# Kernel optimization log

Measured on AMD Instinct MI355X. Metric: run time of the kernel, lower is better.

Reference implementation:

```python
import jax, jax.numpy as jnp
import numpy as np

HD, IN_SZ, V, OP_SZ = 1024, 1024, 400, 128
B, K, L = 64, 8, 13


def log1mexp(x):
    # log(1 - exp(x)) for x <= 0, numerically stable on both ends
    x = jnp.minimum(x, -1e-38)
    big = x > -0.6931472
    return jnp.where(big,
                     jnp.log(-jnp.expm1(jnp.where(big, x, -1.0))),
                     jnp.log1p(-jnp.exp(jnp.where(big, -1.0, x))))


def compute_log_R(log_p, num_points=1000):
    # Unordered-sample ratios for Plackett-Luce sampling without replacement
    # (Kool et al.). P(S) = (1 - p_S) * int_0^1 u^{-p_S} prod_{j in S}(1 - u^{p_j}) du;
    # the (1 - p_S) prefactor cancels in all ratios. Midpoint rule in log-space.
    p = jnp.exp(log_p)                                   # (B,k)
    p_S = jnp.sum(p, axis=-1, keepdims=True)             # (B,1)
    u = (jnp.arange(num_points, dtype=log_p.dtype) + 0.5) / num_points
    log_u = jnp.log(u)                                   # (N,)
    T = log1mexp(p[:, None, :] * log_u[None, :, None])   # (B,N,k): log(1-u^{p_j})
    base = -p_S * log_u[None, :] + jnp.sum(T, axis=-1)   # (B,N)
    logN = jnp.log(jnp.float32(num_points))
    logI = jax.nn.logsumexp(base, axis=-1) - logN        # (B,)   log I(S)
    logI_s = jax.nn.logsumexp(base[:, :, None] - T, axis=1) - logN   # (B,k)
    log_R_s = logI_s - logI[:, None]
    pair = base[:, :, None, None] - T[:, :, :, None] - T[:, :, None, :]  # (B,N,k,k)
    logI_ss = jax.nn.logsumexp(pair, axis=1) - logN      # (B,k,k)
    kk = log_p.shape[-1]
    log_R_ss = jnp.where(jnp.eye(kk, dtype=bool)[None], 0.0,
                         logI_ss - logI_s[:, :, None])
    return log_R_s, log_R_ss


def gumbel_with_maximum(phi, T, u):
    # Gumbel(phi) sample conditioned on its max over axis 1 equaling T (shape (R,1))
    gmb = -jnp.log(-jnp.log(u * (1.0 - 2e-7) + 1e-7))
    g_phi = phi + gmb
    Z = jnp.max(g_phi, axis=1, keepdims=True)
    v = T - g_phi + log1mexp(g_phi - Z)
    return T - jax.nn.relu(v) - jnp.log1p(jnp.exp(-jnp.abs(v)))


def forward(x_feat, W_in_op, b_in_op, W_ih, W_hh, b_ih, b_hh,
            W_fc1, b_fc1, W_out, b_out, gumbel_u, program_len, k):
    Bn = x_feat.shape[0]
    k = int(k)
    program_len = int(program_len)
    Vn = W_out.shape[0]
    H = W_hh.shape[1]
    R = Bn * k
    # beam-major layout: row j*Bn + i is beam j of batch element i (torch split/cat order)
    x_f = jnp.tile(x_feat, (k, 1))                       # (R, in_sz)
    rows = jnp.arange(R)
    batch_idx = jnp.tile(jnp.arange(Bn), k)
    chunk = jnp.arange(k * Vn) // Vn

    def to_beams(z):  # (R, d) -> (Bn, k*d); = torch.cat(torch.split(z, Bn, 0), 1)
        return z.reshape(k, Bn, -1).transpose(1, 0, 2).reshape(Bn, -1)

    def step(carry, xt):
        h, c, G, logp, temp, samples, outputs, ent_plot, entropy_element = carry
        u_t, t = xt
        inp_op = jax.nn.relu(temp @ W_in_op.T + b_in_op)             # (R,128)
        xin = jnp.concatenate([x_f, inp_op], axis=1)                 # (R,in+128)
        gates = xin @ W_ih.T + b_ih + h @ W_hh.T + b_hh              # (R,4H)
        i_g, f_g, g_g, o_g = jnp.split(gates, 4, axis=1)             # torch LSTM order
        c = jax.nn.sigmoid(f_g) * c + jax.nn.sigmoid(i_g) * jnp.tanh(g_g)
        h = jax.nn.sigmoid(o_g) * jnp.tanh(c)
        hd = jax.nn.relu(h @ W_fc1.T + b_fc1)
        logits = hd @ W_out.T + b_out                                # (R,V)
        log_probs = jax.nn.log_softmax(logits, axis=1)
        probs = jax.nn.softmax(logits, axis=1)
        # ---- stochastic-beam-search SWOR step (selection carries no gradient) ----
        phi = jax.lax.stop_gradient(log_probs + logp)
        g = jax.lax.stop_gradient(gumbel_with_maximum(phi, G, u_t))
        nub = jnp.where(t == 0, 1, k)   # unique parent beams (all identical at t=0)
        g2 = jnp.where(chunk[None, :] < nub, to_beams(g), -jnp.inf)  # (Bn,k*V)
        g_val, index = jax.lax.top_k(g2, k)                          # (Bn,k)
        G_new = g_val.T.reshape(R, 1)
        sample = (index % Vn).T.reshape(R)                           # action ids
        order = (index // Vn).T.reshape(R) * Bn + batch_idx          # parent rows
        log_probs = log_probs[order]
        probs = probs[order]
        logp = logp[order] + log_probs[rows, sample][:, None]
        samples = samples[order].at[:, t].set(sample.astype(samples.dtype))
        outputs = outputs[order].at[:, t].set(log_probs[rows, sample])
        h = h[order]
        c = c[order]
        ent = jnp.sum(log_probs * probs, axis=1, keepdims=True)      # (R,1)
        phi_k = to_beams(logp)                                       # (Bn,k)
        log_R_s, log_R_ss = compute_log_R(phi_k)
        w_p_q = jax.lax.stop_gradient(jnp.exp(phi_k + log_R_s))
        Wsum = jnp.sum(w_p_q, axis=1)
        ws = jnp.sum(w_p_q * to_beams(ent), axis=1)
        ent_plot = ent_plot + ws
        entropy_element = entropy_element + ws / Wsum
        temp = jax.nn.one_hot(sample, Vn + 1, dtype=x_feat.dtype)
        new_carry = (h, c, G_new, logp, temp, samples, outputs, ent_plot, entropy_element)
        return new_carry, (log_R_s, log_R_ss, phi_k)

    z = jnp.zeros
    init = (z((R, H)), z((R, H)), z((R, 1)), z((R, 1)),
            jax.nn.one_hot(jnp.full((R,), Vn), Vn + 1, dtype=x_feat.dtype),
            z((R, program_len)), z((R, program_len)), z((Bn,)), z((Bn,)))
    carry, ys = jax.lax.scan(step, init, (gumbel_u, jnp.arange(program_len)))
    samples, outputs, ent_plot, entropy_element = carry[5], carry[6], carry[7], carry[8]
    log_R_s, log_R_ss, phi_k = ys[0][-1], ys[1][-1], ys[2][-1]
    return (to_beams(outputs), to_beams(samples), entropy_element,
            log_R_s, log_R_ss, phi_k, ent_plot)


def setup_inputs() -> dict:
    key = jax.random.key(0)
    ks = jax.random.split(key, 7)

    def lin(kk, out_f, in_f):  # torch nn.Linear default init
        s = 1.0 / np.sqrt(in_f)
        kw, kb = jax.random.split(kk)
        return (jax.random.uniform(kw, (out_f, in_f), jnp.float32, -s, s),
                jax.random.uniform(kb, (out_f,), jnp.float32, -s, s))

    W_in_op, b_in_op = lin(ks[0], OP_SZ, V + 1)
    W_ih, b_ih = lin(ks[1], 4 * HD, IN_SZ + OP_SZ)
    W_hh, b_hh = lin(ks[2], 4 * HD, HD)
    W_fc1, b_fc1 = lin(ks[3], HD, HD)
    W_out, b_out = lin(ks[4], V, HD)
    x_feat = jax.random.normal(ks[5], (B, IN_SZ), jnp.float32)
    gumbel_u = jax.random.uniform(ks[6], (L, B * K, V), jnp.float32)
    return {"x_feat": x_feat, "W_in_op": W_in_op, "b_in_op": b_in_op,
            "W_ih": W_ih, "W_hh": W_hh, "b_ih": b_ih, "b_hh": b_hh,
            "W_fc1": W_fc1, "b_fc1": b_fc1, "W_out": W_out, "b_out": b_out,
            "gumbel_u": gumbel_u, "program_len": L, "k": K}


def reference(x_feat, W_in_op, b_in_op, W_ih, W_hh, b_ih, b_hh,
              W_fc1, b_fc1, W_out, b_out, gumbel_u, program_len, k):
    return forward(x_feat, W_in_op, b_in_op, W_ih, W_hh, b_ih, b_hh,
                   W_fc1, b_fc1, W_out, b_out, gumbel_u, program_len, k)
```

## Files before the change

kernel.cpp:

```cpp
#include <hip/hip_runtime.h>
#include <hip/hip_bf16.h>
#include <cstdint>

#define RR 512
#define KB_ 8
#define VV 400
#define HD_ 1024
#define GD 4096
#define LL 13
#define BKT 16
#define NPTS 1000
#define OUT_N 18560
#define LDP 68
#define AP 36
#define BP 132

__device__ __constant__ int cPJ[28] = {0,0,0,0,0,0,0,1,1,1,1,1,1,2,2,2,2,2,3,3,3,3,4,4,4,5,5,6};
__device__ __constant__ int cPL[28] = {1,2,3,4,5,6,7,2,3,4,5,6,7,3,4,5,6,7,4,5,6,7,5,6,7,6,7,7};

__device__ __forceinline__ float r9_log1mexp(float x) {
  x = fminf(x, -1e-38f);
  return (x > -0.6931472f) ? logf(-expm1f(x)) : log1pf(-expf(x));
}

__device__ __forceinline__ float r9_sigm(float x) { return 1.f / (1.f + expf(-x)); }

__device__ __forceinline__ int r9_pidx(int j, int l) {
  if (j > l) { int t = j; j = l; l = t; }
  return 9 + (j * (15 - j)) / 2 + (l - j - 1);
}

__device__ __forceinline__ float r9_bmax256(float v, float* red) {
  #pragma unroll
  for (int o = 32; o; o >>= 1) v = fmaxf(v, __shfl_xor(v, o, 64));
  __syncthreads();
  if ((threadIdx.x & 63) == 0) red[threadIdx.x >> 6] = v;
  __syncthreads();
  return fmaxf(fmaxf(red[0], red[1]), fmaxf(red[2], red[3]));
}

__device__ __forceinline__ float r9_bsum256(float v, float* red) {
  #pragma unroll
  for (int o = 32; o; o >>= 1) v += __shfl_xor(v, o, 64);
  __syncthreads();
  if ((threadIdx.x & 63) == 0) red[threadIdx.x >> 6] = v;
  __syncthreads();
  return (red[0] + red[1]) + (red[2] + red[3]);
}

__device__ __forceinline__ void r9_gemm(
    const float* __restrict__ A, int lda,
    const float* __restrict__ W, int ldw,
    int K, int r0, int n0, int nmax,
    float (&acc)[4][4], float (*As)[LDP], float (*Bs)[LDP])
{
  const int tid = threadIdx.x;
  const int la = tid >> 2;
  const int lk = (tid & 3) << 2;
  const int tx = tid & 15, ty = tid >> 4;
  for (int k0 = 0; k0 < K; k0 += BKT) {
    float4 av = *reinterpret_cast<const float4*>(A + (size_t)(r0 + la) * lda + (k0 + lk));
    float4 bv = make_float4(0.f, 0.f, 0.f, 0.f);
    if (n0 + la < nmax)
      bv = *reinterpret_cast<const float4*>(W + (size_t)(n0 + la) * ldw + (k0 + lk));
    __syncthreads();
    As[lk + 0][la] = av.x; As[lk + 1][la] = av.y; As[lk + 2][la] = av.z; As[lk + 3][la] = av.w;
    Bs[lk + 0][la] = bv.x; Bs[lk + 1][la] = bv.y; Bs[lk + 2][la] = bv.z; Bs[lk + 3][la] = bv.w;
    __syncthreads();
    #pragma unroll
    for (int kk = 0; kk < BKT; ++kk) {
      float4 a = *reinterpret_cast<const float4*>(&As[kk][ty * 4]);
      float4 b = *reinterpret_cast<const float4*>(&Bs[kk][tx * 4]);
      float ar[4] = {a.x, a.y, a.z, a.w};
      float br[4] = {b.x, b.y, b.z, b.w};
      #pragma unroll
      for (int i = 0; i < 4; ++i)
        #pragma unroll
        for (int j = 0; j < 4; ++j)
          acc[i][j] = fmaf(ar[i], br[j], acc[i][j]);
    }
  }
}

__global__ __launch_bounds__(256) void r9_wszero(float* h0, float* c0, float* Gv,
                                                 float* logp0, float* accum) {
  int idx = blockIdx.x * 256 + threadIdx.x;
  if (idx < RR * HD_) { h0[idx] = 0.f; c0[idx] = 0.f; }
  if (idx < RR) { Gv[idx] = 0.f; logp0[idx] = 0.f; }
  if (idx < 128) accum[idx] = 0.f;
}

__global__ __launch_bounds__(256) void r9_flag(float* dout) {
  int idx = blockIdx.x * 256 + threadIdx.x;
  if (idx < OUT_N) dout[idx] = (idx == 6656) ? 20000.0f : 0.0f;
}

__global__ __launch_bounds__(256) void r9_xfb(const float* __restrict__ xf,
                                              const float* __restrict__ Wih,
                                              const float* __restrict__ bih,
                                              const float* __restrict__ bhh,
                                              float* __restrict__ xfb) {
  __shared__ __align__(16) float As[BKT][LDP];
  __shared__ __align__(16) float Bs[BKT][LDP];
  float acc[4][4] = {};
  int n0 = blockIdx.x * 64;
  r9_gemm(xf, 1024, Wih, 1152, 1024, 0, n0, 1 << 30, acc, As, Bs);
  int tx = threadIdx.x & 15, ty = threadIdx.x >> 4;
  #pragma unroll
  for (int i = 0; i < 4; ++i)
    #pragma unroll
    for (int j = 0; j < 4; ++j) {
      int r = ty * 4 + i, c = n0 + tx * 4 + j;
      xfb[(size_t)r * GD + c] = acc[i][j] + bih[c] + bhh[c];
    }
}

__global__ __launch_bounds__(256) void r9_glstm(
    const float* __restrict__ hprev,
    const float* __restrict__ Whh, const float* __restrict__ Wih,
    const float* __restrict__ Wio, const float* __restrict__ bio,
    const int* __restrict__ s_arr, const int* __restrict__ o_arr, int t,
    float* __restrict__ gates)
{
  __shared__ __align__(16) float As[BKT][AP];
  __shared__ __align__(16) float Bs[BKT][BP];
  float acc[4][4] = {};
  const int tid = threadIdx.x;
  const int c0 = blockIdx.x * 128;
  const int r0 = blockIdx.y * 32;
  const int g  = blockIdx.z;
  const int a_r = tid >> 3;
  const int a_k = (tid & 7) * 2;
  const int b_r = tid >> 1;
  const int b_k = (tid & 1) * 8;
  const int tx = tid & 31, ty = tid >> 5;
  const int arow = r0 + a_r;
  const int asrc = (t == 0) ? arow : o_arr[(size_t)(t - 1) * RR + arow];
  const int s_row = (t == 0) ? 400 : s_arr[(size_t)(t - 1) * RR + arow];
  const float* Arow  = hprev + (size_t)asrc * HD_;
  const float* BrowW = Whh + (size_t)(g * 1024 + c0 + b_r) * HD_;
  for (int k0 = 0; k0 < HD_; k0 += BKT) {
    float2 av = *reinterpret_cast<const float2*>(Arow + k0 + a_k);
    float4 b0 = *reinterpret_cast<const float4*>(BrowW + k0 + b_k);
    float4 b1 = *reinterpret_cast<const float4*>(BrowW + k0 + b_k + 4);
    __syncthreads();
    As[a_k][a_r] = av.x; As[a_k + 1][a_r] = av.y;
    Bs[b_k + 0][b_r] = b0.x; Bs[b_k + 1][b_r] = b0.y;
    Bs[b_k + 2][b_r] = b0.z; Bs[b_k + 3][b_r] = b0.w;
    Bs[b_k + 4][b_r] = b1.x; Bs[b_k + 5][b_r] = b1.y;
    Bs[b_k + 6][b_r] = b1.z; Bs[b_k + 7][b_r] = b1.w;
    __syncthreads();
    #pragma unroll
    for (int kk = 0; kk < BKT; ++kk) {
      float4 a = *reinterpret_cast<const float4*>(&As[kk][ty * 4]);
      float4 b = *reinterpret_cast<const float4*>(&Bs[kk][tx * 4]);
      float ar[4] = {a.x, a.y, a.z, a.w};
      float br[4] = {b.x, b.y, b.z, b.w};
      #pragma unroll
      for (int i = 0; i < 4; ++i)
        #pragma unroll
        for (int j = 0; j < 4; ++j)
          acc[i][j] = fmaf(ar[i], br[j], acc[i][j]);
    }
  }
  const float* BrowI = Wih + (size_t)(g * 1024 + c0 + b_r) * 1152 + 1024;
  for (int k0 = 0; k0 < 128; k0 += BKT) {
    int m0 = k0 + a_k;
    float a0 = fmaxf(Wio[(size_t)m0 * 401 + s_row] + bio[m0], 0.f);
    float a1 = fmaxf(Wio[(size_t)(m0 + 1) * 401 + s_row] + bio[m0 + 1], 0.f);
    float4 b0 = *reinterpret_cast<const float4*>(BrowI + k0 + b_k);
    float4 b1 = *reinterpret_cast<const float4*>(BrowI + k0 + b_k + 4);
    __syncthreads();
    As[a_k][a_r] = a0; As[a_k + 1][a_r] = a1;
    Bs[b_k + 0][b_r] = b0.x; Bs[b_k + 1][b_r] = b0.y;
    Bs[b_k + 2][b_r] = b0.z; Bs[b_k + 3][b_r] = b0.w;
    Bs[b_k + 4][b_r] = b1.x; Bs[b_k + 5][b_r] = b1.y;
    Bs[b_k + 6][b_r] = b1.z; Bs[b_k + 7][b_r] = b1.w;
    __syncthreads();
    #pragma unroll
    for (int kk = 0; kk < BKT; ++kk) {
      float4 a = *reinterpret_cast<const float4*>(&As[kk][ty * 4]);
      float4 b = *reinterpret_cast<const float4*>(&Bs[kk][tx * 4]);
      float ar[4] = {a.x, a.y, a.z, a.w};
      float br[4] = {b.x, b.y, b.z, b.w};
      #pragma unroll
      for (int i = 0; i < 4; ++i)
        #pragma unroll
        for (int j = 0; j < 4; ++j)
          acc[i][j] = fmaf(ar[i], br[j], acc[i][j]);
    }
  }
  #pragma unroll
  for (int i = 0; i < 4; ++i)
    #pragma unroll
    for (int j = 0; j < 4; ++j)
      gates[(size_t)(r0 + ty * 4 + i) * GD + g * 1024 + c0 + tx * 4 + j] = acc[i][j];
}

__global__ __launch_bounds__(256) void r9_lstm(const float* gates, const float* xfb,
                                               const float* cprev, const int* o_arr, int t,
                                               float* cout, float* hout) {
  int idx = blockIdx.x * 256 + threadIdx.x;
  int r = idx >> 10, n = idx & 1023;
  int src = (t == 0) ? r : o_arr[(size_t)(t - 1) * RR + r];
  const float* g = gates + (size_t)r * GD;
  const float* xb = xfb + (size_t)(r & 63) * GD;
  float gi = g[n] + xb[n];
  float gf = g[1024 + n] + xb[1024 + n];
  float gg = g[2048 + n] + xb[2048 + n];
  float go = g[3072 + n] + xb[3072 + n];
  float cp = cprev[(size_t)src * HD_ + n];
  float c = r9_sigm(gf) * cp + r9_sigm(gi) * tanhf(gg);
  cout[idx] = c;
  hout[idx] = r9_sigm(go) * tanhf(c);
}

__global__ __launch_bounds__(256) void r9_fc1(const float* h, const float* W1, float* hdp) {
  __shared__ __align__(16) float As[BKT][LDP];
  __shared__ __align__(16) float Bs[BKT][LDP];
  float acc[4][4] = {};
  int n0 = blockIdx.x * 64, r0 = blockIdx.y * 64, z = blockIdx.z;
  r9_gemm(h + z * 512, HD_, W1 + z * 512, HD_, 512, r0, n0, 1 << 30, acc, As, Bs);
  float* dst = hdp + (size_t)z * RR * HD_;
  int tx = threadIdx.x & 15, ty = threadIdx.x >> 4;
  #pragma unroll
  for (int i = 0; i < 4; ++i)
    #pragma unroll
    for (int j = 0; j < 4; ++j)
      dst[(size_t)(r0 + ty * 4 + i) * HD_ + n0 + tx * 4 + j] = acc[i][j];
}

__global__ __launch_bounds__(256) void r9_fc1c(const float* hdp, const float* b1, float* hd) {
  int idx = blockIdx.x * 256 + threadIdx.x;
  hd[idx] = fmaxf(hdp[idx] + hdp[RR * HD_ + idx] + b1[idx & 1023], 0.f);
}

__global__ __launch_bounds__(256) void r9_out(const float* hd, const float* Wo, float* outp) {
  __shared__ __align__(16) float As[BKT][LDP];
  __shared__ __align__(16) float Bs[BKT][LDP];
  float acc[4][4] = {};
  int n0 = blockIdx.x * 64, r0 = blockIdx.y * 64, z = blockIdx.z;
  r9_gemm(hd + z * 256, HD_, Wo + z * 256, HD_, 256, r0, n0, VV, acc, As, Bs);
  float* dst = outp + (size_t)z * RR * VV;
  int tx = threadIdx.x & 15, ty = threadIdx.x >> 4;
  #pragma unroll
  for (int i = 0; i < 4; ++i)
    #pragma unroll
    for (int j = 0; j < 4; ++j) {
      int c = n0 + tx * 4 + j;
      if (c < VV) dst[(size_t)(r0 + ty * 4 + i) * VV + c] = acc[i][j];
    }
}

__global__ __launch_bounds__(256) void r9_soft(const float* outp, const float* bo,
                                               const float* logp_in, const float* Gv,
                                               const float* gum, float* lp, float* gb,
                                               float* entold) {
  __shared__ float red[4];
  int r = blockIdx.x, tid = threadIdx.x;
  bool v1 = (tid + 256) < VV;
  size_t off0 = (size_t)r * VV + tid;
  float l0 = outp[off0] + outp[RR * VV + off0] + outp[2 * RR * VV + off0]
           + outp[3 * RR * VV + off0] + bo[tid];
  float l1 = -INFINITY;
  if (v1) {
    size_t off1 = off0 + 256;
    l1 = outp[off1] + outp[RR * VV + off1] + outp[2 * RR * VV + off1]
       + outp[3 * RR * VV + off1] + bo[tid + 256];
  }
  float m = r9_bmax256(fmaxf(l0, l1), red);
  float e0 = expf(l0 - m), e1 = v1 ? expf(l1 - m) : 0.f;
  float s = r9_bsum256(e0 + e1, red);
  float ls = logf(s);
  float lp0 = l0 - m - ls, lp1 = l1 - m - ls;
  float ent = lp0 * expf(lp0) + (v1 ? lp1 * expf(lp1) : 0.f);
  ent = r9_bsum256(ent, red);
  if (tid == 0) entold[r] = ent;
  float lpr = logp_in[r];
  const float* ur = gum + (size_t)r * VV;
  float gp0, gp1 = -INFINITY;
  { float u = ur[tid];
    gp0 = lp0 + lpr - logf(-logf(u * (1.f - 2e-7f) + 1e-7f)); }
  if (v1) { float u = ur[tid + 256];
            gp1 = lp1 + lpr - logf(-logf(u * (1.f - 2e-7f) + 1e-7f)); }
  float Z = r9_bmax256(fmaxf(gp0, gp1), red);
  float T = Gv[r];
  int i = r & 63, j = r >> 6;
  float* gbr = gb + (size_t)i * (KB_ * VV) + j * VV;
  {
    float vv = T - gp0 + r9_log1mexp(gp0 - Z);
    gbr[tid] = T - fmaxf(vv, 0.f) - log1pf(expf(-fabsf(vv)));
    lp[(size_t)r * VV + tid] = lp0;
  }
  if (v1) {
    float vv = T - gp1 + r9_log1mexp(gp1 - Z);
    gbr[tid + 256] = T - fmaxf(vv, 0.f) - log1pf(expf(-fabsf(vv)));
    lp[(size_t)r * VV + tid + 256] = lp1;
  }
}

__device__ __forceinline__ unsigned long long r9_pack(float v, int c) {
  unsigned u = __float_as_uint(v);
  u = (u & 0x80000000u) ? ~u : (u | 0x80000000u);
  return ((unsigned long long)u << 32) | (unsigned)(0xFFFFFFFFu - (unsigned)c);
}

__global__ __launch_bounds__(256) void r9_topk(const float* gb, int t, float* Gv,
                                               int* s_t, int* o_t, const float* lp,
                                               const float* logp_in, float* logp_out,
                                               const float* entold, float* entbm,
                                               float* lv_t) {
  __shared__ unsigned long long keys[KB_ * VV];
  __shared__ unsigned long long wbest[4];
  __shared__ unsigned long long selK[KB_];
  int i = blockIdx.x, tid = threadIdx.x;
  int lane = tid & 63, wid = tid >> 6;
  int limit = (t == 0) ? VV : KB_ * VV;
  for (int c = tid; c < limit; c += 256)
    keys[c] = r9_pack(gb[(size_t)i * (KB_ * VV) + c], c);
  __syncthreads();
  for (int it = 0; it < KB_; ++it) {
    unsigned long long b = 0ull;
    for (int c = tid; c < limit; c += 256) {
      unsigned long long k = keys[c];
      b = (k > b) ? k : b;
    }
    #pragma unroll
    for (int o = 32; o; o >>= 1) {
      unsigned long long x = __shfl_xor(b, o, 64);
      b = (x > b) ? x : b;
    }
    if (lane == 0) wbest[wid] = b;
    __syncthreads();
    unsigned long long g = wbest[0];
    g = (wbest[1] > g) ? wbest[1] : g;
    g = (wbest[2] > g) ? wbest[2] : g;
    g = (wbest[3] > g) ? wbest[3] : g;
    if (tid == 0) {
      int csel = (int)(0xFFFFFFFFu - (unsigned)(g & 0xFFFFFFFFu));
      keys[csel] = 0ull;
      selK[it] = g;
    }
    __syncthreads();
  }
  if (tid < KB_) {
    unsigned long long g = selK[tid];
    unsigned x = (unsigned)(g >> 32);
    x = (x & 0x80000000u) ? (x & 0x7FFFFFFFu) : ~x;
    float v = __uint_as_float(x);
    int c = (int)(0xFFFFFFFFu - (unsigned)(g & 0xFFFFFFFFu));
    int r = tid * 64 + i;
    int s = c % VV;
    int o = (c / VV) * 64 + i;
    Gv[r] = v;
    s_t[r] = s;
    o_t[r] = o;
    float lv = lp[(size_t)o * VV + s];
    logp_out[r] = logp_in[o] + lv;
    entbm[r] = entold[o];
    lv_t[r] = lv;
  }
}

__global__ __launch_bounds__(256) void r9_logR(const float* logp_new, const float* entbm,
                                               float* accum, float* dout, int last) {
  __shared__ float Tm[KB_][NPTS];
  __shared__ float base[NPTS];
  __shared__ float phi[KB_], pj[KB_];
  __shared__ float res[37];
  int i = blockIdx.x, tid = threadIdx.x;
  int lane = tid & 63, wid = tid >> 6;
  if (tid < KB_) { float ph = logp_new[tid * 64 + i]; phi[tid] = ph; pj[tid] = expf(ph); }
  __syncthreads();
  float pS = ((pj[0] + pj[1]) + (pj[2] + pj[3])) + ((pj[4] + pj[5]) + (pj[6] + pj[7]));
  for (int n = tid; n < NPTS; n += 256) {
    float lu = logf((n + 0.5f) * (1.0f / NPTS));
    float b = -pS * lu;
    #pragma unroll
    for (int j = 0; j < KB_; ++j) {
      float tv = r9_log1mexp(pj[j] * lu);
      Tm[j][n] = tv; b += tv;
    }
    base[n] = b;
  }
  __syncthreads();
  const float logN = 6.9077552789821f;
  for (int ridx = wid; ridx < 37; ridx += 4) {
    int jj = -1, ll = -1;
    if (ridx >= 1 && ridx < 9) jj = ridx - 1;
    else if (ridx >= 9) { jj = cPJ[ridx - 9]; ll = cPL[ridx - 9]; }
    float mx = -INFINITY;
    for (int n = lane; n < NPTS; n += 64) {
      float v = base[n];
      if (jj >= 0) v -= Tm[jj][n];
      if (ll >= 0) v -= Tm[ll][n];
      mx = fmaxf(mx, v);
    }
    #pragma unroll
    for (int o = 32; o; o >>= 1) mx = fmaxf(mx, __shfl_xor(mx, o, 64));
    float sm = 0.f;
    for (int n = lane; n < NPTS; n += 64) {
      float v = base[n];
      if (jj >= 0) v -= Tm[jj][n];
      if (ll >= 0) v -= Tm[ll][n];
      sm += expf(v - mx);
    }
    #pragma unroll
    for (int o = 32; o; o >>= 1) sm += __shfl_xor(sm, o, 64);
    if (lane == 0) res[ridx] = mx + logf(sm) - logN;
  }
  __syncthreads();
  if (tid == 0) {
    float logI = res[0];
    float Wsum = 0.f, ws = 0.f;
    #pragma unroll
    for (int j = 0; j < KB_; ++j) {
      float lRs = res[1 + j] - logI;
      float wj = expf(phi[j] + lRs);
      Wsum += wj;
      ws += wj * entbm[j * 64 + i];
    }
    accum[i] += ws;
    accum[64 + i] += ws / Wsum;
    if (last) {
      for (int j = 0; j < KB_; ++j) {
        dout[13376 + i * 8 + j] = res[1 + j] - logI;
        dout[17984 + i * 8 + j] = phi[j];
        for (int l = 0; l < KB_; ++l) {
          float v = (l == j) ? 0.f : (res[r9_pidx(j, l)] - res[1 + j]);
          dout[13888 + i * 64 + j * 8 + l] = v;
        }
      }
    }
  }
}

__global__ __launch_bounds__(512) void r9_final(const float* lv_arr, const int* s_arr,
                                                const int* o_arr, const float* accum,
                                                float* dout) {
  int r = threadIdx.x;
  int i = r & 63, j = r >> 6;
  float vals[LL]; int svs[LL];
  int a = r;
  for (int tt = LL - 1; tt >= 0; --tt) {
    vals[tt] = lv_arr[tt * RR + a];
    svs[tt]  = s_arr[tt * RR + a];
    a = o_arr[tt * RR + a];
  }
  #pragma unroll
  for (int tt = 0; tt < LL; ++tt) {
    dout[i * 104 + j * 13 + tt] = vals[tt];
    dout[6656 + i * 104 + j * 13 + tt] = (float)svs[tt];
  }
  if (r < 64) {
    dout[13312 + r] = accum[64 + r];
    dout[18496 + r] = accum[r];
  }
}

extern "C" void kernel_launch(void* const* d_in, const int* in_sizes, int n_in,
                              void* d_out, int out_size, void* d_ws, size_t ws_size,
                              hipStream_t stream) {
  const float* x_feat  = (const float*)d_in[0];
  const float* W_in_op = (const float*)d_in[1];
  const float* b_in_op = (const float*)d_in[2];
  const float* W_ih    = (const float*)d_in[3];
  const float* W_hh    = (const float*)d_in[4];
  const float* b_ih    = (const float*)d_in[5];
  const float* b_hh    = (const float*)d_in[6];
  const float* W_fc1   = (const float*)d_in[7];
  const float* b_fc1   = (const float*)d_in[8];
  const float* W_out   = (const float*)d_in[9];
  const float* b_out   = (const float*)d_in[10];
  const float* gum     = (const float*)d_in[11];
  float* out           = (float*)d_out;

  float* W = (float*)d_ws;
  size_t o = 0;
  float* lv_arr = W + o; o += (size_t)LL * RR;
  float* Gv     = W + o; o += RR;
  float* logpb0 = W + o; o += RR;
  float* logpb1 = W + o; o += RR;
  float* entold = W + o; o += RR;
  float* entbm  = W + o; o += RR;
  float* accum  = W + o; o += 128;
  int* s_arr = (int*)(W + o); o += (size_t)LL * RR;
  int* o_arr = (int*)(W + o); o += (size_t)LL * RR;
  float* xfb    = W + o; o += (size_t)64 * GD;
  float* gates  = W + o; o += (size_t)RR * GD;
  float* lp     = W + o; o += (size_t)RR * VV;
  float* gb     = W + o; o += (size_t)RR * VV;
  float* h2[2]; h2[0] = W + o; o += (size_t)RR * HD_; h2[1] = W + o; o += (size_t)RR * HD_;
  float* c2[2]; c2[0] = W + o; o += (size_t)RR * HD_; c2[1] = W + o; o += (size_t)RR * HD_;
  float* hd     = W + o; o += (size_t)RR * HD_;
  size_t needed_bytes = o * sizeof(float);
  float* logpb[2] = {logpb0, logpb1};
  float* hdp  = gates;
  float* outp = gates;

  if (ws_size < needed_bytes) {
    r9_flag<<<(OUT_N + 255) / 256, 256, 0, stream>>>(out);
    return;
  }

  r9_wszero<<<2048, 256, 0, stream>>>(h2[0], c2[0], Gv, logpb[0], accum);
  r9_xfb<<<64, 256, 0, stream>>>(x_feat, W_ih, b_ih, b_hh, xfb);

  for (int t = 0; t < LL; ++t) {
    int pi = t & 1, po = pi ^ 1;
    r9_glstm<<<dim3(8, 16, 4), 256, 0, stream>>>(h2[pi], W_hh, W_ih, W_in_op, b_in_op,
                                                 s_arr, o_arr, t, gates);
    r9_lstm<<<2048, 256, 0, stream>>>(gates, xfb, c2[pi], o_arr, t, c2[po], h2[po]);
    r9_fc1<<<dim3(16, 8, 2), 256, 0, stream>>>(h2[po], W_fc1, hdp);
    r9_fc1c<<<2048, 256, 0, stream>>>(hdp, b_fc1, hd);
    r9_out<<<dim3(7, 8, 4), 256, 0, stream>>>(hd, W_out, outp);
    r9_soft<<<512, 256, 0, stream>>>(outp, b_out, logpb[pi], Gv,
                                     gum + (size_t)t * RR * VV, lp, gb, entold);
    r9_topk<<<64, 256, 0, stream>>>(gb, t, Gv, s_arr + (size_t)t * RR,
                                    o_arr + (size_t)t * RR, lp, logpb[pi], logpb[po],
                                    entold, entbm, lv_arr + (size_t)t * RR);
    r9_logR<<<64, 256, 0, stream>>>(logpb[po], entbm, accum, out, (t == LL - 1) ? 1 : 0);
  }
  r9_final<<<1, 512, 0, stream>>>(lv_arr, s_arr, o_arr, accum, out);
}
```

Measured before the change: 2.758 ms.

## Retile GEMMs to 4x8 microtiles and fuse softmax, top-k and logR per batch

The LSTM-gate, fc1 and output GEMMs move to 128-thread blocks with 4x8 register microtiles, vectorised A loads and float4 stores. The fc1 bias+ReLU combine is folded into the output GEMM's A-load, removing a separate kernel and its buffer. Softmax, Gumbel sampling, top-k selection and the log-R integration are merged into one kernel per batch element that keeps log-probs and Gumbel keys in shared memory. This cuts launches and global round-trips, but the fused kernel runs only 64 blocks, and the new GEMM tiling halves threads per block.

```diff
diff --git a/kernel.cpp b/kernel.cpp
--- a/kernel.cpp
+++ b/kernel.cpp
@@ -12,57 +12,62 @@
 #define NPTS 1000
 #define OUT_N 18560
 #define LDP 68
-#define AP 36
-#define BP 132
 
 __device__ __constant__ int cPJ[28] = {0,0,0,0,0,0,0,1,1,1,1,1,1,2,2,2,2,2,3,3,3,3,4,4,4,5,5,6};
 __device__ __constant__ int cPL[28] = {1,2,3,4,5,6,7,2,3,4,5,6,7,3,4,5,6,7,4,5,6,7,5,6,7,6,7,7};
 
-__device__ __forceinline__ float r9_log1mexp(float x) {
+__device__ __forceinline__ float rA_log1mexp(float x) {
   x = fminf(x, -1e-38f);
   return (x > -0.6931472f) ? logf(-expm1f(x)) : log1pf(-expf(x));
 }
 
-__device__ __forceinline__ float r9_sigm(float x) { return 1.f / (1.f + expf(-x)); }
-
-__device__ __forceinline__ int r9_pidx(int j, int l) {
+__device__ __forceinline__ float rA_sigm(float x) { return 1.f / (1.f + expf(-x)); }
+
+__device__ __forceinline__ int rA_pidx(int j, int l) {
   if (j > l) { int t = j; j = l; l = t; }
   return 9 + (j * (15 - j)) / 2 + (l - j - 1);
 }
 
-__device__ __forceinline__ float r9_bmax256(float v, float* red) {
+__device__ __forceinline__ float rA_wmax(float v) {
   #pragma unroll
   for (int o = 32; o; o >>= 1) v = fmaxf(v, __shfl_xor(v, o, 64));
-  __syncthreads();
-  if ((threadIdx.x & 63) == 0) red[threadIdx.x >> 6] = v;
-  __syncthreads();
-  return fmaxf(fmaxf(red[0], red[1]), fmaxf(red[2], red[3]));
-}
-
-__device__ __forceinline__ float r9_bsum256(float v, float* red) {
+  return v;
+}
+
+__device__ __forceinline__ float rA_wsum(float v) {
   #pragma unroll
   for (int o = 32; o; o >>= 1) v += __shfl_xor(v, o, 64);
-  __syncthreads();
-  if ((threadIdx.x & 63) == 0) red[threadIdx.x >> 6] = v;
-  __syncthreads();
-  return (red[0] + red[1]) + (red[2] + red[3]);
-}
-
-__device__ __forceinline__ void r9_gemm(
-    const float* __restrict__ A, int lda,
-    const float* __restrict__ W, int ldw,
-    int K, int r0, int n0, int nmax,
-    float (&acc)[4][4], float (*As)[LDP], float (*Bs)[LDP])
-{
+  return v;
+}
+
+__global__ __launch_bounds__(256) void rA_wszero(float* h0, float* c0, float* Gv,
+                                                 float* logp0, float* accum) {
+  int idx = blockIdx.x * 256 + threadIdx.x;
+  if (idx < RR * HD_) { h0[idx] = 0.f; c0[idx] = 0.f; }
+  if (idx < RR) { Gv[idx] = 0.f; logp0[idx] = 0.f; }
+  if (idx < 128) accum[idx] = 0.f;
+}
+
+__global__ __launch_bounds__(256) void rA_flag(float* dout) {
+  int idx = blockIdx.x * 256 + threadIdx.x;
+  if (idx < OUT_N) dout[idx] = (idx == 6656) ? 20000.0f : 0.0f;
+}
+
+__global__ __launch_bounds__(256) void rA_xfb(const float* __restrict__ xf,
+                                              const float* __restrict__ Wih,
+                                              const float* __restrict__ bih,
+                                              const float* __restrict__ bhh,
+                                              float* __restrict__ xfb) {
+  __shared__ __align__(16) float As[BKT][LDP];
+  __shared__ __align__(16) float Bs[BKT][LDP];
+  float acc[4][4] = {};
   const int tid = threadIdx.x;
-  const int la = tid >> 2;
-  const int lk = (tid & 3) << 2;
+  const int n0 = blockIdx.x * 64;
+  const int la = tid >> 2, lk = (tid & 3) << 2;
   const int tx = tid & 15, ty = tid >> 4;
-  for (int k0 = 0; k0 < K; k0 += BKT) {
-    float4 av = *reinterpret_cast<const float4*>(A + (size_t)(r0 + la) * lda + (k0 + lk));
-    float4 bv = make_float4(0.f, 0.f, 0.f, 0.f);
-    if (n0 + la < nmax)
-      bv = *reinterpret_cast<const float4*>(W + (size_t)(n0 + la) * ldw + (k0 + lk));
+  for (int k0 = 0; k0 < 1024; k0 += BKT) {
+    float4 av = *reinterpret_cast<const float4*>(xf + (size_t)la * 1024 + k0 + lk);
+    float4 bv = *reinterpret_cast<const float4*>(Wih + (size_t)(n0 + la) * 1152 + k0 + lk);
     __syncthreads();
     As[lk + 0][la] = av.x; As[lk + 1][la] = av.y; As[lk + 2][la] = av.z; As[lk + 3][la] = av.w;
     Bs[lk + 0][la] = bv.x; Bs[lk + 1][la] = bv.y; Bs[lk + 2][la] = bv.z; Bs[lk + 3][la] = bv.w;
@@ -80,32 +85,6 @@
           acc[i][j] = fmaf(ar[i], br[j], acc[i][j]);
     }
   }
-}
-
-__global__ __launch_bounds__(256) void r9_wszero(float* h0, float* c0, float* Gv,
-                                                 float* logp0, float* accum) {
-  int idx = blockIdx.x * 256 + threadIdx.x;
-  if (idx < RR * HD_) { h0[idx] = 0.f; c0[idx] = 0.f; }
-  if (idx < RR) { Gv[idx] = 0.f; logp0[idx] = 0.f; }
-  if (idx < 128) accum[idx] = 0.f;
-}
-
-__global__ __launch_bounds__(256) void r9_flag(float* dout) {
-  int idx = blockIdx.x * 256 + threadIdx.x;
-  if (idx < OUT_N) dout[idx] = (idx == 6656) ? 20000.0f : 0.0f;
-}
-
-__global__ __launch_bounds__(256) void r9_xfb(const float* __restrict__ xf,
-                                              const float* __restrict__ Wih,
-                                              const float* __restrict__ bih,
-                                              const float* __restrict__ bhh,
-                                              float* __restrict__ xfb) {
-  __shared__ __align__(16) float As[BKT][LDP];
-  __shared__ __align__(16) float Bs[BKT][LDP];
-  float acc[4][4] = {};
-  int n0 = blockIdx.x * 64;
-  r9_gemm(xf, 1024, Wih, 1152, 1024, 0, n0, 1 << 30, acc, As, Bs);
-  int tx = threadIdx.x & 15, ty = threadIdx.x >> 4;
   #pragma unroll
   for (int i = 0; i < 4; ++i)
     #pragma unroll
@@ -115,89 +94,92 @@
     }
 }
 
-__global__ __launch_bounds__(256) void r9_glstm(
+__global__ __launch_bounds__(128) void rA_glstm(
     const float* __restrict__ hprev,
     const float* __restrict__ Whh, const float* __restrict__ Wih,
     const float* __restrict__ Wio, const float* __restrict__ bio,
     const int* __restrict__ s_arr, const int* __restrict__ o_arr, int t,
     float* __restrict__ gates)
 {
-  __shared__ __align__(16) float As[BKT][AP];
-  __shared__ __align__(16) float Bs[BKT][BP];
-  float acc[4][4] = {};
+  __shared__ __align__(16) float As[BKT][LDP];
+  __shared__ __align__(16) float Bs[BKT][LDP];
+  float acc[4][8] = {};
   const int tid = threadIdx.x;
-  const int c0 = blockIdx.x * 128;
-  const int r0 = blockIdx.y * 32;
+  const int c0 = blockIdx.x * 64;
+  const int r0 = blockIdx.y * 64;
   const int g  = blockIdx.z;
-  const int a_r = tid >> 3;
-  const int a_k = (tid & 7) * 2;
-  const int b_r = tid >> 1;
-  const int b_k = (tid & 1) * 8;
-  const int tx = tid & 31, ty = tid >> 5;
-  const int arow = r0 + a_r;
+  const int sr = tid >> 1;
+  const int sk = (tid & 1) * 8;
+  const int tx = tid & 7, ty = tid >> 3;
+  const int arow = r0 + sr;
   const int asrc = (t == 0) ? arow : o_arr[(size_t)(t - 1) * RR + arow];
   const int s_row = (t == 0) ? 400 : s_arr[(size_t)(t - 1) * RR + arow];
-  const float* Arow  = hprev + (size_t)asrc * HD_;
-  const float* BrowW = Whh + (size_t)(g * 1024 + c0 + b_r) * HD_;
+  const float* Arow = hprev + (size_t)asrc * HD_;
+  const float* Brow = Whh + (size_t)(g * 1024 + c0 + sr) * HD_;
   for (int k0 = 0; k0 < HD_; k0 += BKT) {
-    float2 av = *reinterpret_cast<const float2*>(Arow + k0 + a_k);
-    float4 b0 = *reinterpret_cast<const float4*>(BrowW + k0 + b_k);
-    float4 b1 = *reinterpret_cast<const float4*>(BrowW + k0 + b_k + 4);
-    __syncthreads();
-    As[a_k][a_r] = av.x; As[a_k + 1][a_r] = av.y;
-    Bs[b_k + 0][b_r] = b0.x; Bs[b_k + 1][b_r] = b0.y;
-    Bs[b_k + 2][b_r] = b0.z; Bs[b_k + 3][b_r] = b0.w;
-    Bs[b_k + 4][b_r] = b1.x; Bs[b_k + 5][b_r] = b1.y;
-    Bs[b_k + 6][b_r] = b1.z; Bs[b_k + 7][b_r] = b1.w;
+    float4 a0 = *reinterpret_cast<const float4*>(Arow + k0 + sk);
+    float4 a1 = *reinterpret_cast<const float4*>(Arow + k0 + sk + 4);
+    float4 b0 = *reinterpret_cast<const float4*>(Brow + k0 + sk);
+    float4 b1 = *reinterpret_cast<const float4*>(Brow + k0 + sk + 4);
+    __syncthreads();
+    As[sk + 0][sr] = a0.x; As[sk + 1][sr] = a0.y; As[sk + 2][sr] = a0.z; As[sk + 3][sr] = a0.w;
+    As[sk + 4][sr] = a1.x; As[sk + 5][sr] = a1.y; As[sk + 6][sr] = a1.z; As[sk + 7][sr] = a1.w;
+    Bs[sk + 0][sr] = b0.x; Bs[sk + 1][sr] = b0.y; Bs[sk + 2][sr] = b0.z; Bs[sk + 3][sr] = b0.w;
+    Bs[sk + 4][sr] = b1.x; Bs[sk + 5][sr] = b1.y; Bs[sk + 6][sr] = b1.z; Bs[sk + 7][sr] = b1.w;
     __syncthreads();
     #pragma unroll
     for (int kk = 0; kk < BKT; ++kk) {
       float4 a = *reinterpret_cast<const float4*>(&As[kk][ty * 4]);
-      float4 b = *reinterpret_cast<const float4*>(&Bs[kk][tx * 4]);
+      float4 bA = *reinterpret_cast<const float4*>(&Bs[kk][tx * 8]);
+      float4 bB = *reinterpret_cast<const float4*>(&Bs[kk][tx * 8 + 4]);
       float ar[4] = {a.x, a.y, a.z, a.w};
-      float br[4] = {b.x, b.y, b.z, b.w};
+      float br[8] = {bA.x, bA.y, bA.z, bA.w, bB.x, bB.y, bB.z, bB.w};
       #pragma unroll
       for (int i = 0; i < 4; ++i)
         #pragma unroll
-        for (int j = 0; j < 4; ++j)
+        for (int j = 0; j < 8; ++j)
           acc[i][j] = fmaf(ar[i], br[j], acc[i][j]);
     }
   }
-  const float* BrowI = Wih + (size_t)(g * 1024 + c0 + b_r) * 1152 + 1024;
+  const float* BrowI = Wih + (size_t)(g * 1024 + c0 + sr) * 1152 + 1024;
   for (int k0 = 0; k0 < 128; k0 += BKT) {
-    int m0 = k0 + a_k;
-    float a0 = fmaxf(Wio[(size_t)m0 * 401 + s_row] + bio[m0], 0.f);
-    float a1 = fmaxf(Wio[(size_t)(m0 + 1) * 401 + s_row] + bio[m0 + 1], 0.f);
-    float4 b0 = *reinterpret_cast<const float4*>(BrowI + k0 + b_k);
-    float4 b1 = *reinterpret_cast<const float4*>(BrowI + k0 + b_k + 4);
-    __syncthreads();
-    As[a_k][a_r] = a0; As[a_k + 1][a_r] = a1;
-    Bs[b_k + 0][b_r] = b0.x; Bs[b_k + 1][b_r] = b0.y;
-    Bs[b_k + 2][b_r] = b0.z; Bs[b_k + 3][b_r] = b0.w;
-    Bs[b_k + 4][b_r] = b1.x; Bs[b_k + 5][b_r] = b1.y;
-    Bs[b_k + 6][b_r] = b1.z; Bs[b_k + 7][b_r] = b1.w;
+    float av[8];
+    #pragma unroll
+    for (int m = 0; m < 8; ++m) {
+      int mm = k0 + sk + m;
+      av[m] = fmaxf(Wio[(size_t)mm * 401 + s_row] + bio[mm], 0.f);
+    }
+    float4 b0 = *reinterpret_cast<const float4*>(BrowI + k0 + sk);
+    float4 b1 = *reinterpret_cast<const float4*>(BrowI + k0 + sk + 4);
+    __syncthreads();
+    #pragma unroll
+    for (int m = 0; m < 8; ++m) As[sk + m][sr] = av[m];
+    Bs[sk + 0][sr] = b0.x; Bs[sk + 1][sr] = b0.y; Bs[sk + 2][sr] = b0.z; Bs[sk + 3][sr] = b0.w;
+    Bs[sk + 4][sr] = b1.x; Bs[sk + 5][sr] = b1.y; Bs[sk + 6][sr] = b1.z; Bs[sk + 7][sr] = b1.w;
     __syncthreads();
     #pragma unroll
     for (int kk = 0; kk < BKT; ++kk) {
       float4 a = *reinterpret_cast<const float4*>(&As[kk][ty * 4]);
-      float4 b = *reinterpret_cast<const float4*>(&Bs[kk][tx * 4]);
+      float4 bA = *reinterpret_cast<const float4*>(&Bs[kk][tx * 8]);
+      float4 bB = *reinterpret_cast<const float4*>(&Bs[kk][tx * 8 + 4]);
       float ar[4] = {a.x, a.y, a.z, a.w};
-      float br[4] = {b.x, b.y, b.z, b.w};
+      float br[8] = {bA.x, bA.y, bA.z, bA.w, bB.x, bB.y, bB.z, bB.w};
       #pragma unroll
       for (int i = 0; i < 4; ++i)
         #pragma unroll
-        for (int j = 0; j < 4; ++j)
+        for (int j = 0; j < 8; ++j)
           acc[i][j] = fmaf(ar[i], br[j], acc[i][j]);
     }
   }
   #pragma unroll
-  for (int i = 0; i < 4; ++i)
-    #pragma unroll
-    for (int j = 0; j < 4; ++j)
-      gates[(size_t)(r0 + ty * 4 + i) * GD + g * 1024 + c0 + tx * 4 + j] = acc[i][j];
-}
-
-__global__ __launch_bounds__(256) void r9_lstm(const float* gates, const float* xfb,
+  for (int i = 0; i < 4; ++i) {
+    float* dst = gates + (size_t)(r0 + ty * 4 + i) * GD + g * 1024 + c0 + tx * 8;
+    *reinterpret_cast<float4*>(dst) = make_float4(acc[i][0], acc[i][1], acc[i][2], acc[i][3]);
+    *reinterpret_cast<float4*>(dst + 4) = make_float4(acc[i][4], acc[i][5], acc[i][6], acc[i][7]);
+  }
+}
+
+__global__ __launch_bounds__(256) void rA_lstm(const float* gates, const float* xfb,
                                                const float* cprev, const int* o_arr, int t,
                                                float* cout, float* hout) {
   int idx = blockIdx.x * 256 + threadIdx.x;
@@ -210,119 +192,204 @@
   float gg = g[2048 + n] + xb[2048 + n];
   float go = g[3072 + n] + xb[3072 + n];
   float cp = cprev[(size_t)src * HD_ + n];
-  float c = r9_sigm(gf) * cp + r9_sigm(gi) * tanhf(gg);
+  float c = rA_sigm(gf) * cp + rA_sigm(gi) * tanhf(gg);
   cout[idx] = c;
-  hout[idx] = r9_sigm(go) * tanhf(c);
-}
-
-__global__ __launch_bounds__(256) void r9_fc1(const float* h, const float* W1, float* hdp) {
+  hout[idx] = rA_sigm(go) * tanhf(c);
+}
+
+__global__ __launch_bounds__(128) void rA_fc1(const float* __restrict__ h,
+                                              const float* __restrict__ W1, float* hdp) {
   __shared__ __align__(16) float As[BKT][LDP];
   __shared__ __align__(16) float Bs[BKT][LDP];
-  float acc[4][4] = {};
-  int n0 = blockIdx.x * 64, r0 = blockIdx.y * 64, z = blockIdx.z;
-  r9_gemm(h + z * 512, HD_, W1 + z * 512, HD_, 512, r0, n0, 1 << 30, acc, As, Bs);
-  float* dst = hdp + (size_t)z * RR * HD_;
-  int tx = threadIdx.x & 15, ty = threadIdx.x >> 4;
-  #pragma unroll
-  for (int i = 0; i < 4; ++i)
-    #pragma unroll
-    for (int j = 0; j < 4; ++j)
-      dst[(size_t)(r0 + ty * 4 + i) * HD_ + n0 + tx * 4 + j] = acc[i][j];
-}
-
-__global__ __launch_bounds__(256) void r9_fc1c(const float* hdp, const float* b1, float* hd) {
-  int idx = blockIdx.x * 256 + threadIdx.x;
-  hd[idx] = fmaxf(hdp[idx] + hdp[RR * HD_ + idx] + b1[idx & 1023], 0.f);
-}
-
-__global__ __launch_bounds__(256) void r9_out(const float* hd, const float* Wo, float* outp) {
+  float acc[4][8] = {};
+  const int tid = threadIdx.x;
+  const int n0 = blockIdx.x * 64, r0 = blockIdx.y * 64, z = blockIdx.z;
+  const int sr = tid >> 1, sk = (tid & 1) * 8;
+  const int tx = tid & 7, ty = tid >> 3;
+  const float* Arow = h + (size_t)(r0 + sr) * HD_ + z * 512;
+  const float* Brow = W1 + (size_t)(n0 + sr) * HD_ + z * 512;
+  for (int k0 = 0; k0 < 512; k0 += BKT) {
+    float4 a0 = *reinterpret_cast<const float4*>(Arow + k0 + sk);
+    float4 a1 = *reinterpret_cast<const float4*>(Arow + k0 + sk + 4);
+    float4 b0 = *reinterpret_cast<const float4*>(Brow + k0 + sk);
+    float4 b1 = *reinterpret_cast<const float4*>(Brow + k0 + sk + 4);
+    __syncthreads();
+    As[sk + 0][sr] = a0.x; As[sk + 1][sr] = a0.y; As[sk + 2][sr] = a0.z; As[sk + 3][sr] = a0.w;
+    As[sk + 4][sr] = a1.x; As[sk + 5][sr] = a1.y; As[sk + 6][sr] = a1.z; As[sk + 7][sr] = a1.w;
+    Bs[sk + 0][sr] = b0.x; Bs[sk + 1][sr] = b0.y; Bs[sk + 2][sr] = b0.z; Bs[sk + 3][sr] = b0.w;
+    Bs[sk + 4][sr] = b1.x; Bs[sk + 5][sr] = b1.y; Bs[sk + 6][sr] = b1.z; Bs[sk + 7][sr] = b1.w;
+    __syncthreads();
+    #pragma unroll
+    for (int kk = 0; kk < BKT; ++kk) {
+      float4 a = *reinterpret_cast<const float4*>(&As[kk][ty * 4]);
+      float4 bA = *reinterpret_cast<const float4*>(&Bs[kk][tx * 8]);
+      float4 bB = *reinterpret_cast<const float4*>(&Bs[kk][tx * 8 + 4]);
+      float ar[4] = {a.x, a.y, a.z, a.w};
+      float br[8] = {bA.x, bA.y, bA.z, bA.w, bB.x, bB.y, bB.z, bB.w};
+      #pragma unroll
+      for (int i = 0; i < 4; ++i)
+        #pragma unroll
+        for (int j = 0; j < 8; ++j)
+          acc[i][j] = fmaf(ar[i], br[j], acc[i][j]);
+    }
+  }
+  float* base = hdp + (size_t)z * RR * HD_;
+  #pragma unroll
+  for (int i = 0; i < 4; ++i) {
+    float* dst = base + (size_t)(r0 + ty * 4 + i) * HD_ + n0 + tx * 8;
+    *reinterpret_cast<float4*>(dst) = make_float4(acc[i][0], acc[i][1], acc[i][2], acc[i][3]);
+    *reinterpret_cast<float4*>(dst + 4) = make_float4(acc[i][4], acc[i][5], acc[i][6], acc[i][7]);
+  }
+}
+
+__global__ __launch_bounds__(128) void rA_out(const float* __restrict__ hdp,
+                                              const float* __restrict__ b1,
+                                              const float* __restrict__ Wo, float* outp) {
   __shared__ __align__(16) float As[BKT][LDP];
   __shared__ __align__(16) float Bs[BKT][LDP];
-  float acc[4][4] = {};
-  int n0 = blockIdx.x * 64, r0 = blockIdx.y * 64, z = blockIdx.z;
-  r9_gemm(hd + z * 256, HD_, Wo + z * 256, HD_, 256, r0, n0, VV, acc, As, Bs);
-  float* dst = outp + (size_t)z * RR * VV;
-  int tx = threadIdx.x & 15, ty = threadIdx.x >> 4;
+  float acc[4][8] = {};
+  const int tid = threadIdx.x;
+  const int n0 = blockIdx.x * 64, r0 = blockIdx.y * 64, z = blockIdx.z;
+  const int sr = tid >> 1, sk = (tid & 1) * 8;
+  const int tx = tid & 7, ty = tid >> 3;
+  const size_t arow_off = (size_t)(r0 + sr) * HD_ + z * 256;
+  const int bcol = n0 + sr;
+  const float* Brow = Wo + (size_t)bcol * HD_ + z * 256;
+  for (int k0 = 0; k0 < 256; k0 += BKT) {
+    float av[8];
+    #pragma unroll
+    for (int m = 0; m < 8; ++m) {
+      int kg = z * 256 + k0 + sk + m;
+      av[m] = fmaxf(hdp[arow_off + k0 + sk + m] + hdp[RR * HD_ + arow_off + k0 + sk + m]
+                    + b1[kg], 0.f);
+    }
+    float4 b0 = make_float4(0.f, 0.f, 0.f, 0.f), b1v = b0;
+    if (bcol < VV) {
+      b0  = *reinterpret_cast<const float4*>(Brow + k0 + sk);
+      b1v = *reinterpret_cast<const float4*>(Brow + k0 + sk + 4);
+    }
+    __syncthreads();
+    #pragma unroll
+    for (int m = 0; m < 8; ++m) As[sk + m][sr] = av[m];
+    Bs[sk + 0][sr] = b0.x; Bs[sk + 1][sr] = b0.y; Bs[sk + 2][sr] = b0.z; Bs[sk + 3][sr] = b0.w;
+    Bs[sk + 4][sr] = b1v.x; Bs[sk + 5][sr] = b1v.y; Bs[sk + 6][sr] = b1v.z; Bs[sk + 7][sr] = b1v.w;
+    __syncthreads();
+    #pragma unroll
+    for (int kk = 0; kk < BKT; ++kk) {
+      float4 a = *reinterpret_cast<const float4*>(&As[kk][ty * 4]);
+      float4 bA = *reinterpret_cast<const float4*>(&Bs[kk][tx * 8]);
+      float4 bB = *reinterpret_cast<const float4*>(&Bs[kk][tx * 8 + 4]);
+      float ar[4] = {a.x, a.y, a.z, a.w};
+      float br[8] = {bA.x, bA.y, bA.z, bA.w, bB.x, bB.y, bB.z, bB.w};
+      #pragma unroll
+      for (int i = 0; i < 4; ++i)
+        #pragma unroll
+        for (int j = 0; j < 8; ++j)
+          acc[i][j] = fmaf(ar[i], br[j], acc[i][j]);
+    }
+  }
+  float* base = outp + (size_t)z * RR * VV;
   #pragma unroll
   for (int i = 0; i < 4; ++i)
     #pragma unroll
-    for (int j = 0; j < 4; ++j) {
-      int c = n0 + tx * 4 + j;
-      if (c < VV) dst[(size_t)(r0 + ty * 4 + i) * VV + c] = acc[i][j];
-    }
-}
-
-__global__ __launch_bounds__(256) void r9_soft(const float* outp, const float* bo,
-                                               const float* logp_in, const float* Gv,
-                                               const float* gum, float* lp, float* gb,
-                                               float* entold) {
-  __shared__ float red[4];
-  int r = blockIdx.x, tid = threadIdx.x;
-  bool v1 = (tid + 256) < VV;
-  size_t off0 = (size_t)r * VV + tid;
-  float l0 = outp[off0] + outp[RR * VV + off0] + outp[2 * RR * VV + off0]
-           + outp[3 * RR * VV + off0] + bo[tid];
-  float l1 = -INFINITY;
-  if (v1) {
-    size_t off1 = off0 + 256;
-    l1 = outp[off1] + outp[RR * VV + off1] + outp[2 * RR * VV + off1]
-       + outp[3 * RR * VV + off1] + bo[tid + 256];
-  }
-  float m = r9_bmax256(fmaxf(l0, l1), red);
-  float e0 = expf(l0 - m), e1 = v1 ? expf(l1 - m) : 0.f;
-  float s = r9_bsum256(e0 + e1, red);
-  float ls = logf(s);
-  float lp0 = l0 - m - ls, lp1 = l1 - m - ls;
-  float ent = lp0 * expf(lp0) + (v1 ? lp1 * expf(lp1) : 0.f);
-  ent = r9_bsum256(ent, red);
-  if (tid == 0) entold[r] = ent;
-  float lpr = logp_in[r];
-  const float* ur = gum + (size_t)r * VV;
-  float gp0, gp1 = -INFINITY;
-  { float u = ur[tid];
-    gp0 = lp0 + lpr - logf(-logf(u * (1.f - 2e-7f) + 1e-7f)); }
-  if (v1) { float u = ur[tid + 256];
-            gp1 = lp1 + lpr - logf(-logf(u * (1.f - 2e-7f) + 1e-7f)); }
-  float Z = r9_bmax256(fmaxf(gp0, gp1), red);
-  float T = Gv[r];
-  int i = r & 63, j = r >> 6;
-  float* gbr = gb + (size_t)i * (KB_ * VV) + j * VV;
-  {
-    float vv = T - gp0 + r9_log1mexp(gp0 - Z);
-    gbr[tid] = T - fmaxf(vv, 0.f) - log1pf(expf(-fabsf(vv)));
-    lp[(size_t)r * VV + tid] = lp0;
-  }
-  if (v1) {
-    float vv = T - gp1 + r9_log1mexp(gp1 - Z);
-    gbr[tid + 256] = T - fmaxf(vv, 0.f) - log1pf(expf(-fabsf(vv)));
-    lp[(size_t)r * VV + tid + 256] = lp1;
-  }
-}
-
-__device__ __forceinline__ unsigned long long r9_pack(float v, int c) {
+    for (int j = 0; j < 8; ++j) {
+      int c = n0 + tx * 8 + j;
+      if (c < VV) base[(size_t)(r0 + ty * 4 + i) * VV + c] = acc[i][j];
+    }
+}
+
+__device__ __forceinline__ unsigned long long rA_pack(float v, int c) {
   unsigned u = __float_as_uint(v);
   u = (u & 0x80000000u) ? ~u : (u | 0x80000000u);
   return ((unsigned long long)u << 32) | (unsigned)(0xFFFFFFFFu - (unsigned)c);
 }
 
-__global__ __launch_bounds__(256) void r9_topk(const float* gb, int t, float* Gv,
-                                               int* s_t, int* o_t, const float* lp,
-                                               const float* logp_in, float* logp_out,
-                                               const float* entold, float* entbm,
-                                               float* lv_t) {
-  __shared__ unsigned long long keys[KB_ * VV];
-  __shared__ unsigned long long wbest[4];
-  __shared__ unsigned long long selK[KB_];
-  int i = blockIdx.x, tid = threadIdx.x;
-  int lane = tid & 63, wid = tid >> 6;
+__global__ __launch_bounds__(256) void rA_smax(
+    const float* __restrict__ outp, const float* __restrict__ bo,
+    const float* __restrict__ logp_in, float* logp_out, float* Gv,
+    const float* __restrict__ gum, int* s_t, int* o_t, float* lv_t,
+    float* accum, float* dout, int t, int last)
+{
+  __shared__ __align__(16) float shbuf[9000];
+  __shared__ float entold8[KB_], phi8[KB_], entb8[KB_], pj8[KB_];
+  __shared__ float res[37];
+  __shared__ unsigned long long wbest[4], selK[KB_];
+  float* gk  = shbuf;
+  float* lpl = shbuf + 3200;
+  const int i = blockIdx.x, tid = threadIdx.x;
+  const int lane = tid & 63, wid = tid >> 6;
+
+  for (int rl = wid; rl < KB_; rl += 4) {
+    int r = rl * 64 + i;
+    float lv_[7];
+    float m = -INFINITY;
+    #pragma unroll
+    for (int ch = 0; ch < 7; ++ch) {
+      int n = ch * 64 + lane;
+      float l = -INFINITY;
+      if (n < VV) {
+        size_t off = (size_t)r * VV + n;
+        l = outp[off] + outp[RR * VV + off] + outp[2 * RR * VV + off]
+          + outp[3 * RR * VV + off] + bo[n];
+      }
+      lv_[ch] = l;
+      m = fmaxf(m, l);
+    }
+    m = rA_wmax(m);
+    float ssum = 0.f;
+    #pragma unroll
+    for (int ch = 0; ch < 7; ++ch) {
+      int n = ch * 64 + lane;
+      if (n < VV) ssum += expf(lv_[ch] - m);
+    }
+    ssum = rA_wsum(ssum);
+    float ls = logf(ssum);
+    float ent = 0.f;
+    #pragma unroll
+    for (int ch = 0; ch < 7; ++ch) {
+      int n = ch * 64 + lane;
+      if (n < VV) {
+        float lp = lv_[ch] - m - ls;
+        lpl[rl * VV + n] = lp;
+        ent += lp * expf(lp);
+        lv_[ch] = lp;
+      }
+    }
+    ent = rA_wsum(ent);
+    if (lane == 0) entold8[rl] = ent;
+    float lpr = logp_in[r];
+    const float* ur = gum + (size_t)r * VV;
+    float gp_[7];
+    float Z = -INFINITY;
+    #pragma unroll
+    for (int ch = 0; ch < 7; ++ch) {
+      int n = ch * 64 + lane;
+      float gp = -INFINITY;
+      if (n < VV) {
+        float u = ur[n];
+        gp = lv_[ch] + lpr - logf(-logf(u * (1.f - 2e-7f) + 1e-7f));
+      }
+      gp_[ch] = gp;
+      Z = fmaxf(Z, gp);
+    }
+    Z = rA_wmax(Z);
+    float T = Gv[r];
+    #pragma unroll
+    for (int ch = 0; ch < 7; ++ch) {
+      int n = ch * 64 + lane;
+      if (n < VV) {
+        float vv = T - gp_[ch] + rA_log1mexp(gp_[ch] - Z);
+        gk[rl * VV + n] = T - fmaxf(vv, 0.f) - log1pf(expf(-fabsf(vv)));
+      }
+    }
+  }
+  __syncthreads();
+
   int limit = (t == 0) ? VV : KB_ * VV;
-  for (int c = tid; c < limit; c += 256)
-    keys[c] = r9_pack(gb[(size_t)i * (KB_ * VV) + c], c);
-  __syncthreads();
   for (int it = 0; it < KB_; ++it) {
     unsigned long long b = 0ull;
     for (int c = tid; c < limit; c += 256) {
-      unsigned long long k = keys[c];
+      unsigned long long k = rA_pack(gk[c], c);
       b = (k > b) ? k : b;
     }
     #pragma unroll
@@ -338,11 +405,12 @@
     g = (wbest[3] > g) ? wbest[3] : g;
     if (tid == 0) {
       int csel = (int)(0xFFFFFFFFu - (unsigned)(g & 0xFFFFFFFFu));
-      keys[csel] = 0ull;
+      gk[csel] = -INFINITY;
       selK[it] = g;
     }
     __syncthreads();
   }
+
   if (tid < KB_) {
     unsigned long long g = selK[tid];
     unsigned x = (unsigned)(g >> 32);
@@ -351,34 +419,30 @@
     int c = (int)(0xFFFFFFFFu - (unsigned)(g & 0xFFFFFFFFu));
     int r = tid * 64 + i;
     int s = c % VV;
-    int o = (c / VV) * 64 + i;
+    int jp = c / VV;
+    int o = jp * 64 + i;
     Gv[r] = v;
     s_t[r] = s;
     o_t[r] = o;
-    float lv = lp[(size_t)o * VV + s];
-    logp_out[r] = logp_in[o] + lv;
-    entbm[r] = entold[o];
+    float lv = lpl[jp * VV + s];
+    float ph = logp_in[o] + lv;
+    logp_out[r] = ph;
     lv_t[r] = lv;
-  }
-}
-
-__global__ __launch_bounds__(256) void r9_logR(const float* logp_new, const float* entbm,
-                                               float* accum, float* dout, int last) {
-  __shared__ float Tm[KB_][NPTS];
-  __shared__ float base[NPTS];
-  __shared__ float phi[KB_], pj[KB_];
-  __shared__ float res[37];
-  int i = blockIdx.x, tid = threadIdx.x;
-  int lane = tid & 63, wid = tid >> 6;
-  if (tid < KB_) { float ph = logp_new[tid * 64 + i]; phi[tid] = ph; pj[tid] = expf(ph); }
+    phi8[tid] = ph;
+    pj8[tid] = expf(ph);
+    entb8[tid] = entold8[jp];
+  }
   __syncthreads();
-  float pS = ((pj[0] + pj[1]) + (pj[2] + pj[3])) + ((pj[4] + pj[5]) + (pj[6] + pj[7]));
+
+  float (*Tm)[NPTS] = reinterpret_cast<float (*)[NPTS]>(shbuf);
+  float* base = shbuf + 8000;
+  float pS = ((pj8[0] + pj8[1]) + (pj8[2] + pj8[3])) + ((pj8[4] + pj8[5]) + (pj8[6] + pj8[7]));
   for (int n = tid; n < NPTS; n += 256) {
     float lu = logf((n + 0.5f) * (1.0f / NPTS));
     float b = -pS * lu;
     #pragma unroll
     for (int j = 0; j < KB_; ++j) {
-      float tv = r9_log1mexp(pj[j] * lu);
+      float tv = rA_log1mexp(pj8[j] * lu);
       Tm[j][n] = tv; b += tv;
     }
     base[n] = b;
@@ -396,8 +460,7 @@
       if (ll >= 0) v -= Tm[ll][n];
       mx = fmaxf(mx, v);
     }
-    #pragma unroll
-    for (int o = 32; o; o >>= 1) mx = fmaxf(mx, __shfl_xor(mx, o, 64));
+    mx = rA_wmax(mx);
     float sm = 0.f;
     for (int n = lane; n < NPTS; n += 64) {
       float v = base[n];
@@ -405,8 +468,7 @@
       if (ll >= 0) v -= Tm[ll][n];
       sm += expf(v - mx);
     }
-    #pragma unroll
-    for (int o = 32; o; o >>= 1) sm += __shfl_xor(sm, o, 64);
+    sm = rA_wsum(sm);
     if (lane == 0) res[ridx] = mx + logf(sm) - logN;
   }
   __syncthreads();
@@ -416,18 +478,18 @@
     #pragma unroll
     for (int j = 0; j < KB_; ++j) {
       float lRs = res[1 + j] - logI;
-      float wj = expf(phi[j] + lRs);
+      float wj = expf(phi8[j] + lRs);
       Wsum += wj;
-      ws += wj * entbm[j * 64 + i];
+      ws += wj * entb8[j];
     }
     accum[i] += ws;
     accum[64 + i] += ws / Wsum;
     if (last) {
       for (int j = 0; j < KB_; ++j) {
         dout[13376 + i * 8 + j] = res[1 + j] - logI;
-        dout[17984 + i * 8 + j] = phi[j];
+        dout[17984 + i * 8 + j] = phi8[j];
         for (int l = 0; l < KB_; ++l) {
-          float v = (l == j) ? 0.f : (res[r9_pidx(j, l)] - res[1 + j]);
+          float v = (l == j) ? 0.f : (res[rA_pidx(j, l)] - res[1 + j]);
           dout[13888 + i * 64 + j * 8 + l] = v;
         }
       }
@@ -435,7 +497,7 @@
   }
 }
 
-__global__ __launch_bounds__(512) void r9_final(const float* lv_arr, const int* s_arr,
+__global__ __launch_bounds__(512) void rA_final(const float* lv_arr, const int* s_arr,
                                                 const int* o_arr, const float* accum,
                                                 float* dout) {
   int r = threadIdx.x;
@@ -481,45 +543,38 @@
   float* Gv     = W + o; o += RR;
   float* logpb0 = W + o; o += RR;
   float* logpb1 = W + o; o += RR;
-  float* entold = W + o; o += RR;
-  float* entbm  = W + o; o += RR;
   float* accum  = W + o; o += 128;
   int* s_arr = (int*)(W + o); o += (size_t)LL * RR;
   int* o_arr = (int*)(W + o); o += (size_t)LL * RR;
   float* xfb    = W + o; o += (size_t)64 * GD;
   float* gates  = W + o; o += (size_t)RR * GD;
-  float* lp     = W + o; o += (size_t)RR * VV;
-  float* gb     = W + o; o += (size_t)RR * VV;
   float* h2[2]; h2[0] = W + o; o += (size_t)RR * HD_; h2[1] = W + o; o += (size_t)RR * HD_;
   float* c2[2]; c2[0] = W + o; o += (size_t)RR * HD_; c2[1] = W + o; o += (size_t)RR * HD_;
-  float* hd     = W + o; o += (size_t)RR * HD_;
   size_t needed_bytes = o * sizeof(float);
   float* logpb[2] = {logpb0, logpb1};
   float* hdp  = gates;
-  float* outp = gates;
+  float* outp = gates + (size_t)2 * RR * HD_;
 
   if (ws_size < needed_bytes) {
-    r9_flag<<<(OUT_N + 255) / 256, 256, 0, stream>>>(out);
+    rA_flag<<<(OUT_N + 255) / 256, 256, 0, stream>>>(out);
     return;
   }
 
-  r9_wszero<<<2048, 256, 0, stream>>>(h2[0], c2[0], Gv, logpb[0], accum);
-  r9_xfb<<<64, 256, 0, stream>>>(x_feat, W_ih, b_ih, b_hh, xfb);
+  rA_wszero<<<2048, 256, 0, stream>>>(h2[0], c2[0], Gv, logpb[0], accum);
+  rA_xfb<<<64, 256, 0, stream>>>(x_feat, W_ih, b_ih, b_hh, xfb);
 
   for (int t = 0; t < LL; ++t) {
     int pi = t & 1, po = pi ^ 1;
-    r9_glstm<<<dim3(8, 16, 4), 256, 0, stream>>>(h2[pi], W_hh, W_ih, W_in_op, b_in_op,
+    rA_glstm<<<dim3(16, 8, 4), 128, 0, stream>>>(h2[pi], W_hh, W_ih, W_in_op, b_in_op,
                                                  s_arr, o_arr, t, gates);
-    r9_lstm<<<2048, 256, 0, stream>>>(gates, xfb, c2[pi], o_arr, t, c2[po], h2[po]);
-    r9_fc1<<<dim3(16, 8, 2), 256, 0, stream>>>(h2[po], W_fc1, hdp);
-    r9_fc1c<<<2048, 256, 0, stream>>>(hdp, b_fc1, hd);
-    r9_out<<<dim3(7, 8, 4), 256, 0, stream>>>(hd, W_out, outp);
-    r9_soft<<<512, 256, 0, stream>>>(outp, b_out, logpb[pi], Gv,
-                                     gum + (size_t)t * RR * VV, lp, gb, entold);
-    r9_topk<<<64, 256, 0, stream>>>(gb, t, Gv, s_arr + (size_t)t * RR,
-                                    o_arr + (size_t)t * RR, lp, logpb[pi], logpb[po],
-                                    entold, entbm, lv_arr + (size_t)t * RR);
-    r9_logR<<<64, 256, 0, stream>>>(logpb[po], entbm, accum, out, (t == LL - 1) ? 1 : 0);
-  }
-  r9_final<<<1, 512, 0, stream>>>(lv_arr, s_arr, o_arr, accum, out);
-}
+    rA_lstm<<<2048, 256, 0, stream>>>(gates, xfb, c2[pi], o_arr, t, c2[po], h2[po]);
+    rA_fc1<<<dim3(16, 8, 2), 128, 0, stream>>>(h2[po], W_fc1, hdp);
+    rA_out<<<dim3(7, 8, 4), 128, 0, stream>>>(hdp, b_fc1, W_out, outp);
+    rA_smax<<<64, 256, 0, stream>>>(outp, b_out, logpb[pi], logpb[po], Gv,
+                                    gum + (size_t)t * RR * VV,
+                                    s_arr + (size_t)t * RR, o_arr + (size_t)t * RR,
+                                    lv_arr + (size_t)t * RR, accum, out,
+                                    t, (t == LL - 1) ? 1 : 0);
+  }
+  rA_final<<<1, 512, 0, stream>>>(lv_arr, s_arr, o_arr, accum, out);
+}
```

Result: slower. 3.456 ms (+25.3%).
